# Optimization experiments

Hardware: AMD Instinct MI355X
Metric: run time of the kernel (lower is better)

## Reference

```python
import jax, jax.numpy as jnp
import numpy as np
import math

PS = 8          # patch_size
OUT_C = 16      # out_channels
D_MODEL = 64
P_STATE = 32
BANDLIMIT = 1.0
STEP_SCALE = 1.0  # dt1 reference rate


def _ln(x, g, b, eps=1e-5):
    mu = jnp.mean(x, -1, keepdims=True)
    var = jnp.mean((x - mu) ** 2, -1, keepdims=True)
    return (x - mu) * jax.lax.rsqrt(var + eps) * g + b


def _forward(x, W_embed, b_embed, g1, beta1, Lambda_re, Lambda_im, B_re, B_im,
             C_re, C_im, D, log_step, g2, beta2, W_enc, W_dec, g3, beta3, W_out, b_out):
    b, t, h, w = x.shape
    hp, wp = h // PS, w // PS
    n = hp * wp
    # patchify: [b,t,h,w] -> [b,t,n,ps*ps]
    xp = x.reshape(b, t, hp, PS, wp, PS).transpose(0, 1, 2, 4, 3, 5).reshape(b, t, n, PS * PS)
    xe = xp @ W_embed.T + b_embed                              # [b,t,n,d]
    u = xe.transpose(0, 2, 1, 3).reshape(b * n, t, D_MODEL)    # [(b n), t, d]

    # ---- S5Block: pre-norm -> diagonal SSM -> gelu + residual -> GEGLU FFN ----
    fx = _ln(u, g1, beta1)
    Lam = Lambda_re + 1j * Lambda_im                           # [P] complex eigenvalues
    step = STEP_SCALE * jnp.exp(log_step)                      # [P]
    Lbar = jnp.exp(Lam * step)                                 # ZOH: A_bar
    Bbar = ((Lbar - 1.0) / Lam)[:, None] * (B_re + 1j * B_im)  # ZOH: B_bar [P,d]
    # bandlimit mask on C (freqs = step*|Im(Lambda)|/(2pi) < bandlimit/2)
    freqs = step * jnp.abs(Lambda_im) / (2.0 * math.pi)
    mask = (freqs < BANDLIMIT * 0.5).astype(C_re.dtype)
    Cc = (C_re + 1j * C_im) * mask[None, :]                    # [d,P]

    Bu = jnp.einsum('ntd,pd->ntp', fx.astype(jnp.complex64), Bbar)   # [(bn),t,P]
    A = jnp.broadcast_to(Lbar.astype(jnp.complex64), (1, t, P_STATE))

    def comb(e1, e2):
        a1, b1 = e1
        a2, b2 = e2
        return a1 * a2, a2 * b1 + b2

    _, xs = jax.lax.associative_scan(comb, (A, Bu), axis=1)    # x_k = A*x_{k-1} + Bu_k (x_0 = 0)
    ys = jnp.einsum('ntp,dp->ntd', xs, Cc).real + fx * D       # y = Re(C x) + D u
    xb = jax.nn.gelu(ys, approximate=False) + fx

    fx2 = _ln(xb, g2, beta2)
    enc = fx2 @ W_enc.T                                        # [(bn),t,2d]
    a, gate = jnp.split(enc, 2, axis=-1)
    xb = (a * jax.nn.gelu(gate, approximate=False)) @ W_dec.T + fx2

    # ---- take last timestep, project, unpatchify ----
    x_last = xb[:, -1, :]                                      # [(bn), d]
    proj = _ln(x_last, g3, beta3) @ W_out.T + b_out            # [(bn), C*ps*ps]
    y = proj.reshape(b, hp, wp, OUT_C, PS, PS).transpose(0, 3, 1, 4, 2, 5).reshape(b, OUT_C, h, w)
    return y


def setup_inputs() -> dict:
    key = jax.random.key(0)
    ks = jax.random.split(key, 12)
    d, P, pp = D_MODEL, P_STATE, PS * PS
    return dict(
        x=jax.random.normal(ks[0], (8, 15, 480, 640), jnp.float32),
        W_embed=jax.random.normal(ks[1], (d, pp), jnp.float32) / math.sqrt(pp),
        b_embed=jnp.zeros((d,), jnp.float32),
        g1=jnp.ones((d,), jnp.float32), beta1=jnp.zeros((d,), jnp.float32),
        Lambda_re=-0.5 * jnp.ones((P,), jnp.float32),
        Lambda_im=math.pi * (1.0 + jnp.arange(P, dtype=jnp.float32)),
        B_re=jax.random.normal(ks[2], (P, d), jnp.float32) / math.sqrt(d),
        B_im=jax.random.normal(ks[3], (P, d), jnp.float32) / math.sqrt(d),
        C_re=jax.random.normal(ks[4], (d, P), jnp.float32) / math.sqrt(P),
        C_im=jax.random.normal(ks[5], (d, P), jnp.float32) / math.sqrt(P),
        D=jax.random.normal(ks[6], (d,), jnp.float32),
        log_step=jax.random.uniform(ks[7], (P,), jnp.float32, math.log(1e-3), math.log(1e-1)),
        g2=jnp.ones((d,), jnp.float32), beta2=jnp.zeros((d,), jnp.float32),
        W_enc=jax.random.normal(ks[8], (2 * d, d), jnp.float32) / math.sqrt(d),
        W_dec=jax.random.normal(ks[9], (d, d), jnp.float32) / math.sqrt(d),
        g3=jnp.ones((d,), jnp.float32), beta3=jnp.zeros((d,), jnp.float32),
        W_out=jax.random.normal(ks[10], (OUT_C * pp, d), jnp.float32) / math.sqrt(d),
        b_out=jnp.zeros((OUT_C * pp,), jnp.float32),
    )


def reference(x, W_embed, b_embed, g1, beta1, Lambda_re, Lambda_im, B_re, B_im,
              C_re, C_im, D, log_step, g2, beta2, W_enc, W_dec, g3, beta3, W_out, b_out):
    return _forward(x, W_embed, b_embed, g1, beta1, Lambda_re, Lambda_im, B_re, B_im,
                    C_re, C_im, D, log_step, g2, beta2, W_enc, W_dec, g3, beta3, W_out, b_out)
```

## Files before the change

kernel.cpp:

```cpp
#include <hip/hip_runtime.h>
#include <math.h>


typedef __attribute__((ext_vector_type(8))) short short8;
typedef __attribute__((ext_vector_type(4))) float f32x4;

#define MFMA16(a, b, c) __builtin_amdgcn_mfma_f32_16x16x32_bf16((a), (b), (c), 0, 0, 0)

__device__ __forceinline__ short f2bf(float f) {
  union { float f; unsigned u; } v; v.f = f;
  unsigned r = (v.u + 0x7fffu + ((v.u >> 16) & 1u)) >> 16;
  return (short)r;
}
__device__ __forceinline__ float geluf(float x) {
  return 0.5f * x * (1.0f + erff(x * 0.70710678118654752f));
}
__device__ __forceinline__ short8 packfrag(const f32x4& a, const f32x4& b) {
  short8 o;
  o[0] = f2bf(a[0]); o[1] = f2bf(a[1]); o[2] = f2bf(a[2]); o[3] = f2bf(a[3]);
  o[4] = f2bf(b[0]); o[5] = f2bf(b[1]); o[6] = f2bf(b[2]); o[7] = f2bf(b[3]);
  return o;
}
__device__ __forceinline__ int ecmap(int i, int m) {
  return (i >> 1) * 32 + (m >> 2) * 8 + (i & 1) * 4 + (m & 3);
}
__device__ __forceinline__ int swz(int b) {
  return b ^ (((b >> 2) ^ (b >> 6)) & 0x60) ^ (((b >> 3) ^ (b >> 9)) & 0x10);
}
__device__ __forceinline__ void bbar_factors(const float* Lre, const float* Lim,
                                             const float* lstep, int p,
                                             float& fre, float& fim) {
  float st = expf(lstep[p]);
  float lr = Lre[p], li = Lim[p];
  float er = expf(lr * st);
  float lbr = er * cosf(li * st), lbi = er * sinf(li * st);
  float u = lbr - 1.0f, v = lbi;
  float den = lr * lr + li * li;
  fre = (u * lr + v * li) / den;
  fim = (v * lr - u * li) / den;
}

__global__ __launch_bounds__(256) void k0_prep(
    const float* __restrict__ W_embed, const float* __restrict__ g1,
    const float* __restrict__ be1, const float* __restrict__ Lre,
    const float* __restrict__ Lim, const float* __restrict__ Bre,
    const float* __restrict__ Bim, const float* __restrict__ Cre,
    const float* __restrict__ Cim, const float* __restrict__ lstep,
    const float* __restrict__ W_enc, const float* __restrict__ W_dec,
    const float* __restrict__ W_out, short* __restrict__ wimg,
    float* __restrict__ bu0) {
  const int bid = blockIdx.x;
  if (bid == 44) {
    int q = threadIdx.x;
    if (q < 64) {
      int c = q >> 5, p = q & 31;
      float fre, fim; bbar_factors(Lre, Lim, lstep, p, fre, fim);
      float s = 0.f;
      for (int d = 0; d < 64; ++d) {
        float br = Bre[p * 64 + d], bi = Bim[p * 64 + d];
        float val = c ? (fre * bi + fim * br) : (fre * br - fim * bi);
        s += be1[d] * val;
      }
      bu0[q] = s;
    }
    return;
  }
  const int w = threadIdx.x >> 6, lane = threadIdx.x & 63;
  const int m = lane & 15, qd = lane >> 4;
  const int f = bid * 4 + w;
  short v[8];
  if (f < 8) {
    int i = f >> 1, kt = f & 1, chan = ecmap(i, m), k0 = kt * 32 + qd * 8;
#pragma unroll
    for (int j = 0; j < 8; ++j) v[j] = f2bf(W_embed[chan * 64 + k0 + j]);
  } else if (f < 16) {
    int fi = f - 8, i = fi >> 1, kt = fi & 1;
    int comp = i & 1, p = (i >> 1) * 16 + m, d0 = kt * 32 + qd * 8;
    float fre, fim; bbar_factors(Lre, Lim, lstep, p, fre, fim);
#pragma unroll
    for (int j = 0; j < 8; ++j) {
      int d = d0 + j;
      float br = Bre[p * 64 + d], bi = Bim[p * 64 + d];
      float val = comp ? (fre * bi + fim * br) : (fre * br - fim * bi);
      v[j] = f2bf(g1[d] * val);
    }
  } else if (f < 24) {
    int fi = f - 16, i = fi >> 1, kt = fi & 1, chan = ecmap(i, m);
#pragma unroll
    for (int j = 0; j < 8; ++j) {
      int comp = j >> 2, p = kt * 16 + qd * 4 + (j & 3);
      float stp = expf(lstep[p]);
      float fr = stp * fabsf(Lim[p]) * (1.0f / 6.28318530717958648f);
      float msk = (fr < 0.5f) ? 1.f : 0.f;
      float val = comp ? -Cim[chan * 32 + p] * msk : Cre[chan * 32 + p] * msk;
      v[j] = f2bf(val);
    }
  } else if (f < 40) {
    int fi = f - 24, i = fi >> 1, kt = fi & 1;
    int row = (i < 4) ? ecmap(i, m) : 64 + ecmap(i - 4, m);
#pragma unroll
    for (int j = 0; j < 8; ++j) v[j] = f2bf(W_enc[row * 64 + kt * 32 + qd * 8 + j]);
  } else if (f < 48) {
    int fi = f - 40, i = fi >> 1, kt = fi & 1, row = ecmap(i, m);
#pragma unroll
    for (int j = 0; j < 8; ++j) v[j] = f2bf(W_dec[row * 64 + kt * 32 + qd * 8 + j]);
  } else {
    int fi = f - 48, i = fi >> 1, kt = fi & 1, row = i * 16 + m;
#pragma unroll
    for (int j = 0; j < 8; ++j) v[j] = f2bf(W_out[row * 64 + kt * 32 + qd * 8 + j]);
  }
  short8 sv;
#pragma unroll
  for (int j = 0; j < 8; ++j) sv[j] = v[j];
  *(short8*)&wimg[(f * 64 + lane) * 8] = sv;
}

__global__ __launch_bounds__(256) void k1_fused(
    const float* __restrict__ x, const short* __restrict__ wimg_g,
    const float* __restrict__ bu0_g, const float* __restrict__ Lre,
    const float* __restrict__ Lim, const float* __restrict__ lstep,
    const float* __restrict__ g1, const float* __restrict__ be1,
    const float* __restrict__ bemb, const float* __restrict__ Dv,
    const float* __restrict__ g2, const float* __restrict__ be2,
    float* __restrict__ xlastT) {
  __shared__ __align__(16) char smem[49152];
#define WF(id) (*(const short8*)(smem + (id) * 1024 + lane * 16))

  const int tid = threadIdx.x;
  const int wv = tid >> 6, lane = tid & 63;
  const int s = lane & 15, qd = lane >> 4;

  float4 wreg[4];
  {
    const float4* src = (const float4*)wimg_g;
#pragma unroll
    for (int j = 0; j < 4; ++j) wreg[j] = src[j * 256 + tid];
  }

  int cb[4];
  f32x4 bec[4], bu0c[4];
#pragma unroll
  for (int nt = 0; nt < 4; ++nt) {
    cb[nt] = (nt >> 1) * 32 + qd * 8 + (nt & 1) * 4;
    bec[nt] = *(const f32x4*)(bemb + cb[nt]);
    bu0c[nt] = *(const f32x4*)(bu0_g + (nt & 1) * 32 + (nt >> 1) * 16 + qd * 4);
  }
  f32x4 lbr[2], lbi[2];
#pragma unroll
  for (int k = 0; k < 2; ++k)
#pragma unroll
    for (int r = 0; r < 4; ++r) {
      int p = k * 16 + qd * 4 + r;
      float st = expf(lstep[p]);
      float er = expf(Lre[p] * st);
      lbr[k][r] = er * cosf(Lim[p] * st);
      lbi[k][r] = er * sinf(Lim[p] * st);
    }

  int off[4];
#pragma unroll
  for (int j = 0; j < 4; ++j) {
    int L = (wv * 4 + j) * 1024 + lane * 16;
    int b = swz(L);
    int c = b >> 4;
    int r = c >> 7, p = (c >> 1) & 63, h = c & 1;
    int seq = blockIdx.x * 64 + p;
    int b_i = seq / 4800, pr = seq % 4800;
    int ph = pr / 80, pw = pr % 80;
    off[j] = ((b_i * 15) * 480 + ph * 8 + r) * 640 + pw * 8 + h * 4;
  }
  int rb[4];
#pragma unroll
  for (int kt = 0; kt < 2; ++kt)
#pragma unroll
    for (int h = 0; h < 2; ++h) {
      int b = (kt * 4 + qd) * 2048 + (wv * 16 + s) * 32 + h * 16;
      rb[kt * 2 + h] = swz(b);
    }

#define STAGE(bufofs, tt)                                                     \
  {                                                                           \
    const float* gsrc = x + (tt) * 307200;                                    \
    char* lb = smem + (bufofs) + wv * 4096;                                   \
    _Pragma("unroll") for (int j = 0; j < 4; ++j)                             \
        __builtin_amdgcn_global_load_lds(                                     \
            (const __attribute__((address_space(1))) void*)(gsrc + off[j]),   \
            (__attribute__((address_space(3))) void*)(lb + j * 1024),         \
            16, 0, 0);                                                        \
  }

  const int sbase = (blockIdx.x * 4 + wv) * 16;

  STAGE(16384, 0);
  STAGE(32768, 1);
  {
    float4* wdst = (float4*)smem;
#pragma unroll
    for (int j = 0; j < 4; ++j) wdst[j * 256 + tid] = wreg[j];
  }
  asm volatile("s_waitcnt vmcnt(0) lgkmcnt(0)" ::: "memory");
  __builtin_amdgcn_s_barrier();

  const f32x4 zf = {0.f, 0.f, 0.f, 0.f};
  f32x4 state[4] = {zf, zf, zf, zf};
  f32x4 xh[4];

  for (int t = 0; t < 15; ++t) {
    const char* bufr = smem + 16384 + ((t & 1) << 14);
    f32x4 vcur[4];
#pragma unroll
    for (int q = 0; q < 4; ++q) vcur[q] = *(const f32x4*)(bufr + rb[q]);
    asm volatile("s_waitcnt lgkmcnt(0)" ::: "memory");
    __builtin_amdgcn_s_barrier();
    if (t < 13) STAGE(16384 + ((t & 1) << 14), t + 2);

    short8 pa0 = packfrag(vcur[0], vcur[1]);
    short8 pa1 = packfrag(vcur[2], vcur[3]);
    f32x4 c1[4];
#pragma unroll
    for (int i = 0; i < 4; ++i) {
      f32x4 acc = MFMA16(WF(i * 2), pa0, zf);
      acc = MFMA16(WF(i * 2 + 1), pa1, acc);
      c1[i] = acc + bec[i];
    }
    float sm = 0.f, sq = 0.f;
#pragma unroll
    for (int nt = 0; nt < 4; ++nt)
#pragma unroll
      for (int i = 0; i < 4; ++i) { sm += c1[nt][i]; sq += c1[nt][i] * c1[nt][i]; }
    sm += __shfl_xor(sm, 16); sq += __shfl_xor(sq, 16);
    sm += __shfl_xor(sm, 32); sq += __shfl_xor(sq, 32);
    float mean = sm * 0.015625f;
    float rstd = rsqrtf(sq * 0.015625f - mean * mean + 1e-5f);
#pragma unroll
    for (int nt = 0; nt < 4; ++nt) xh[nt] = (c1[nt] - mean) * rstd;
    short8 xa0 = packfrag(xh[0], xh[1]);
    short8 xa1 = packfrag(xh[2], xh[3]);
#pragma unroll
    for (int k = 0; k < 2; ++k) {
      f32x4 re = state[2 * k], im = state[2 * k + 1];
      state[2 * k]     = lbr[k] * re - lbi[k] * im + bu0c[2 * k];
      state[2 * k + 1] = lbr[k] * im + lbi[k] * re + bu0c[2 * k + 1];
    }
#pragma unroll
    for (int i = 0; i < 4; ++i) {
      state[i] = MFMA16(WF(8 + i * 2), xa0, state[i]);
      state[i] = MFMA16(WF(8 + i * 2 + 1), xa1, state[i]);
    }

    if (t < 14) {
      if (t < 13) asm volatile("s_waitcnt vmcnt(4)" ::: "memory");
      else        asm volatile("s_waitcnt vmcnt(0)" ::: "memory");
      __builtin_amdgcn_s_barrier();
    }
  }
#undef STAGE

  __syncthreads();
  {
    float4 hf[8];
    const float4* src = (const float4*)(wimg_g + 16 * 512);
#pragma unroll
    for (int j = 0; j < 8; ++j) hf[j] = src[j * 256 + tid];
    float4* dst = (float4*)(smem + 16384);
#pragma unroll
    for (int j = 0; j < 8; ++j) dst[j * 256 + tid] = hf[j];
  }
  __syncthreads();

  f32x4 g1c[4], b1c[4], Dc[4], g2c[4], b2c[4];
#pragma unroll
  for (int nt = 0; nt < 4; ++nt) {
    g1c[nt] = *(const f32x4*)(g1 + cb[nt]);
    b1c[nt] = *(const f32x4*)(be1 + cb[nt]);
    Dc[nt] = *(const f32x4*)(Dv + cb[nt]);
    g2c[nt] = *(const f32x4*)(g2 + cb[nt]);
    b2c[nt] = *(const f32x4*)(be2 + cb[nt]);
  }
  f32x4 fxl[4];
#pragma unroll
  for (int nt = 0; nt < 4; ++nt) fxl[nt] = xh[nt] * g1c[nt] + b1c[nt];

  short8 xsa0 = packfrag(state[0], state[1]);
  short8 xsa1 = packfrag(state[2], state[3]);
  f32x4 xbv[4];
#pragma unroll
  for (int i = 0; i < 4; ++i) {
    f32x4 acc = fxl[i] * Dc[i];
    acc = MFMA16(WF(16 + i * 2), xsa0, acc);
    acc = MFMA16(WF(16 + i * 2 + 1), xsa1, acc);
#pragma unroll
    for (int r = 0; r < 4; ++r) xbv[i][r] = geluf(acc[r]) + fxl[i][r];
  }
  float sm2 = 0.f, sq2 = 0.f;
#pragma unroll
  for (int nt = 0; nt < 4; ++nt)
#pragma unroll
    for (int i = 0; i < 4; ++i) { sm2 += xbv[nt][i]; sq2 += xbv[nt][i] * xbv[nt][i]; }
  sm2 += __shfl_xor(sm2, 16); sq2 += __shfl_xor(sq2, 16);
  sm2 += __shfl_xor(sm2, 32); sq2 += __shfl_xor(sq2, 32);
  float mean2 = sm2 * 0.015625f;
  float rstd2 = rsqrtf(sq2 * 0.015625f - mean2 * mean2 + 1e-5f);
  f32x4 fx2[4];
#pragma unroll
  for (int nt = 0; nt < 4; ++nt)
    fx2[nt] = (xbv[nt] - mean2) * rstd2 * g2c[nt] + b2c[nt];

  short8 fa0 = packfrag(fx2[0], fx2[1]);
  short8 fa1 = packfrag(fx2[2], fx2[3]);
  f32x4 e[8];
#pragma unroll
  for (int i = 0; i < 8; ++i) {
    f32x4 acc = MFMA16(WF(24 + i * 2), fa0, zf);
    e[i] = MFMA16(WF(24 + i * 2 + 1), fa1, acc);
  }
  f32x4 hv[4];
#pragma unroll
  for (int nt = 0; nt < 4; ++nt)
#pragma unroll
    for (int i = 0; i < 4; ++i) hv[nt][i] = e[nt][i] * geluf(e[nt + 4][i]);

  short8 ha0 = packfrag(hv[0], hv[1]);
  short8 ha1 = packfrag(hv[2], hv[3]);
  f32x4 xo[4];
#pragma unroll
  for (int i = 0; i < 4; ++i) {
    f32x4 acc = fx2[i];
    acc = MFMA16(WF(40 + i * 2), ha0, acc);
    xo[i] = MFMA16(WF(40 + i * 2 + 1), ha1, acc);
  }
#pragma unroll
  for (int kt = 0; kt < 2; ++kt)
#pragma unroll
    for (int j = 0; j < 8; ++j)
      xlastT[(kt * 32 + qd * 8 + j) * 38400 + sbase + s] = xo[2 * kt + (j >> 2)][j & 3];
#undef WF
}

__global__ __launch_bounds__(256) void k2_head(
    const float* __restrict__ xlastT, const short* __restrict__ wout_img,
    const float* __restrict__ g3, const float* __restrict__ be3,
    const float* __restrict__ b_out, float* __restrict__ y) {
  __shared__ short wo[32 * 512];
  const int nqb = blockIdx.x & 3;
  const int mblk = blockIdx.x >> 2;
  {
    float4* dst = (float4*)wo;
    const float4* src = (const float4*)(wout_img + nqb * 32 * 512);
    for (int i = threadIdx.x; i < 2048; i += 256) dst[i] = src[i];
  }
  __syncthreads();
  const int wv = threadIdx.x >> 6, lane = threadIdx.x & 63;
  const int s = lane & 15, qd = lane >> 4;
  const int sbase = mblk * 64 + wv * 16;
  const int seq = sbase + s;
  const int nq0 = nqb * 256;

  float vals[2][8];
#pragma unroll
  for (int kt = 0; kt < 2; ++kt)
#pragma unroll
    for (int j = 0; j < 8; ++j)
      vals[kt][j] = xlastT[(kt * 32 + qd * 8 + j) * 38400 + seq];
  float sm = 0.f, sq = 0.f;
#pragma unroll
  for (int kt = 0; kt < 2; ++kt)
#pragma unroll
    for (int j = 0; j < 8; ++j) { sm += vals[kt][j]; sq += vals[kt][j] * vals[kt][j]; }
  sm += __shfl_xor(sm, 16); sq += __shfl_xor(sq, 16);
  sm += __shfl_xor(sm, 32); sq += __shfl_xor(sq, 32);
  float mean = sm * 0.015625f;
  float rstd = rsqrtf(sq * 0.015625f - mean * mean + 1e-5f);

  short8 zb[2];
#pragma unroll
  for (int kt = 0; kt < 2; ++kt) {
    f32x4 ga = *(const f32x4*)(g3 + kt * 32 + qd * 8);
    f32x4 gb = *(const f32x4*)(g3 + kt * 32 + qd * 8 + 4);
    f32x4 ba = *(const f32x4*)(be3 + kt * 32 + qd * 8);
    f32x4 bb = *(const f32x4*)(be3 + kt * 32 + qd * 8 + 4);
#pragma unroll
    for (int j = 0; j < 4; ++j) {
      zb[kt][j] = f2bf((vals[kt][j] - mean) * rstd * ga[j] + ba[j]);
      zb[kt][j + 4] = f2bf((vals[kt][j + 4] - mean) * rstd * gb[j] + bb[j]);
    }
  }
  const int bi2 = seq / 4800, prr = seq % 4800;
  const int phh = prr / 80, pww = prr % 80;
  const int obase = (bi2 * 16 * 480 + phh * 8) * 640 + pww * 8;

#pragma unroll
  for (int nt = 0; nt < 16; ++nt) {
    int o0 = nq0 + nt * 16 + qd * 4;
    f32x4 acc = *(const f32x4*)(b_out + o0);
    acc = MFMA16(*(const short8*)&wo[(nt * 2 + 0) * 512 + lane * 8], zb[0], acc);
    acc = MFMA16(*(const short8*)&wo[(nt * 2 + 1) * 512 + lane * 8], zb[1], acc);
    int c = o0 >> 6, pi = (o0 >> 3) & 7, pj = o0 & 7;
    *(f32x4*)&y[obase + c * 307200 + pi * 640 + pj] = acc;
  }
}

extern "C" void kernel_launch(void* const* d_in, const int* in_sizes, int n_in,
                              void* d_out, int out_size, void* d_ws, size_t ws_size,
                              hipStream_t stream) {
  const float* x       = (const float*)d_in[0];
  const float* W_embed = (const float*)d_in[1];
  const float* b_embed = (const float*)d_in[2];
  const float* g1      = (const float*)d_in[3];
  const float* beta1   = (const float*)d_in[4];
  const float* Lre     = (const float*)d_in[5];
  const float* Lim     = (const float*)d_in[6];
  const float* Bre     = (const float*)d_in[7];
  const float* Bim     = (const float*)d_in[8];
  const float* Cre     = (const float*)d_in[9];
  const float* Cim     = (const float*)d_in[10];
  const float* Dv      = (const float*)d_in[11];
  const float* lstep   = (const float*)d_in[12];
  const float* g2      = (const float*)d_in[13];
  const float* beta2   = (const float*)d_in[14];
  const float* W_enc   = (const float*)d_in[15];
  const float* W_dec   = (const float*)d_in[16];
  const float* g3      = (const float*)d_in[17];
  const float* beta3   = (const float*)d_in[18];
  const float* W_out   = (const float*)d_in[19];
  const float* b_out   = (const float*)d_in[20];
  float* y = (float*)d_out;

  short* wimg = (short*)d_ws;
  float* bu0 = (float*)((char*)d_ws + 176 * 1024);
  float* xlastT = (float*)((char*)d_ws + 180 * 1024);

  k0_prep<<<dim3(45), dim3(256), 0, stream>>>(W_embed, g1, beta1, Lre, Lim,
                                              Bre, Bim, Cre, Cim, lstep,
                                              W_enc, W_dec, W_out, wimg, bu0);
  k1_fused<<<dim3(600), dim3(256), 0, stream>>>(x, wimg, bu0, Lre, Lim, lstep,
                                                g1, beta1, b_embed, Dv, g2,
                                                beta2, xlastT);
  k2_head<<<dim3(2400), dim3(256), 0, stream>>>(xlastT, wimg + 48 * 512, g3,
                                                beta3, b_out, y);
}
```

Measured before the change: 342.3 us.

## Fuse final layernorm and output projection head into main SSM kernel

```diff
diff --git a/kernel.cpp b/kernel.cpp
--- a/kernel.cpp
+++ b/kernel.cpp
@@ -122,7 +122,8 @@
     const float* __restrict__ g1, const float* __restrict__ be1,
     const float* __restrict__ bemb, const float* __restrict__ Dv,
     const float* __restrict__ g2, const float* __restrict__ be2,
-    float* __restrict__ xlastT) {
+    const float* __restrict__ g3, const float* __restrict__ be3,
+    const float* __restrict__ b_out, float* __restrict__ y) {
   __shared__ __align__(16) char smem[49152];
 #define WF(id) (*(const short8*)(smem + (id) * 1024 + lane * 16))
 
@@ -329,75 +330,44 @@
     acc = MFMA16(WF(40 + i * 2), ha0, acc);
     xo[i] = MFMA16(WF(40 + i * 2 + 1), ha1, acc);
   }
-#pragma unroll
-  for (int kt = 0; kt < 2; ++kt)
-#pragma unroll
-    for (int j = 0; j < 8; ++j)
-      xlastT[(kt * 32 + qd * 8 + j) * 38400 + sbase + s] = xo[2 * kt + (j >> 2)][j & 3];
-#undef WF
-}
-
-__global__ __launch_bounds__(256) void k2_head(
-    const float* __restrict__ xlastT, const short* __restrict__ wout_img,
-    const float* __restrict__ g3, const float* __restrict__ be3,
-    const float* __restrict__ b_out, float* __restrict__ y) {
-  __shared__ short wo[32 * 512];
-  const int nqb = blockIdx.x & 3;
-  const int mblk = blockIdx.x >> 2;
-  {
-    float4* dst = (float4*)wo;
-    const float4* src = (const float4*)(wout_img + nqb * 32 * 512);
-    for (int i = threadIdx.x; i < 2048; i += 256) dst[i] = src[i];
-  }
-  __syncthreads();
-  const int wv = threadIdx.x >> 6, lane = threadIdx.x & 63;
-  const int s = lane & 15, qd = lane >> 4;
-  const int sbase = mblk * 64 + wv * 16;
+
+  float sm3 = 0.f, sq3 = 0.f;
+#pragma unroll
+  for (int nt = 0; nt < 4; ++nt)
+#pragma unroll
+    for (int i = 0; i < 4; ++i) { sm3 += xo[nt][i]; sq3 += xo[nt][i] * xo[nt][i]; }
+  sm3 += __shfl_xor(sm3, 16); sq3 += __shfl_xor(sq3, 16);
+  sm3 += __shfl_xor(sm3, 32); sq3 += __shfl_xor(sq3, 32);
+  float mean3 = sm3 * 0.015625f;
+  float rstd3 = rsqrtf(sq3 * 0.015625f - mean3 * mean3 + 1e-5f);
+  f32x4 z[4];
+#pragma unroll
+  for (int nt = 0; nt < 4; ++nt) {
+    f32x4 g3c = *(const f32x4*)(g3 + cb[nt]);
+    f32x4 b3c = *(const f32x4*)(be3 + cb[nt]);
+    z[nt] = (xo[nt] - mean3) * rstd3 * g3c + b3c;
+  }
+  short8 za = packfrag(z[0], z[1]);
+  short8 zb = packfrag(z[2], z[3]);
+
   const int seq = sbase + s;
-  const int nq0 = nqb * 256;
-
-  float vals[2][8];
-#pragma unroll
-  for (int kt = 0; kt < 2; ++kt)
-#pragma unroll
-    for (int j = 0; j < 8; ++j)
-      vals[kt][j] = xlastT[(kt * 32 + qd * 8 + j) * 38400 + seq];
-  float sm = 0.f, sq = 0.f;
-#pragma unroll
-  for (int kt = 0; kt < 2; ++kt)
-#pragma unroll
-    for (int j = 0; j < 8; ++j) { sm += vals[kt][j]; sq += vals[kt][j] * vals[kt][j]; }
-  sm += __shfl_xor(sm, 16); sq += __shfl_xor(sq, 16);
-  sm += __shfl_xor(sm, 32); sq += __shfl_xor(sq, 32);
-  float mean = sm * 0.015625f;
-  float rstd = rsqrtf(sq * 0.015625f - mean * mean + 1e-5f);
-
-  short8 zb[2];
-#pragma unroll
-  for (int kt = 0; kt < 2; ++kt) {
-    f32x4 ga = *(const f32x4*)(g3 + kt * 32 + qd * 8);
-    f32x4 gb = *(const f32x4*)(g3 + kt * 32 + qd * 8 + 4);
-    f32x4 ba = *(const f32x4*)(be3 + kt * 32 + qd * 8);
-    f32x4 bb = *(const f32x4*)(be3 + kt * 32 + qd * 8 + 4);
-#pragma unroll
-    for (int j = 0; j < 4; ++j) {
-      zb[kt][j] = f2bf((vals[kt][j] - mean) * rstd * ga[j] + ba[j]);
-      zb[kt][j + 4] = f2bf((vals[kt][j + 4] - mean) * rstd * gb[j] + bb[j]);
-    }
-  }
   const int bi2 = seq / 4800, prr = seq % 4800;
   const int phh = prr / 80, pww = prr % 80;
   const int obase = (bi2 * 16 * 480 + phh * 8) * 640 + pww * 8;
-
-#pragma unroll
-  for (int nt = 0; nt < 16; ++nt) {
-    int o0 = nq0 + nt * 16 + qd * 4;
+  const short* wob = wimg_g + 48 * 512;
+
+#pragma unroll 4
+  for (int ntg = 0; ntg < 64; ++ntg) {
+    short8 a0 = *(const short8*)&wob[(ntg * 2 + 0) * 512 + lane * 8];
+    short8 a1 = *(const short8*)&wob[(ntg * 2 + 1) * 512 + lane * 8];
+    int o0 = ntg * 16 + qd * 4;
     f32x4 acc = *(const f32x4*)(b_out + o0);
-    acc = MFMA16(*(const short8*)&wo[(nt * 2 + 0) * 512 + lane * 8], zb[0], acc);
-    acc = MFMA16(*(const short8*)&wo[(nt * 2 + 1) * 512 + lane * 8], zb[1], acc);
+    acc = MFMA16(a0, za, acc);
+    acc = MFMA16(a1, zb, acc);
     int c = o0 >> 6, pi = (o0 >> 3) & 7, pj = o0 & 7;
     *(f32x4*)&y[obase + c * 307200 + pi * 640 + pj] = acc;
   }
+#undef WF
 }
 
 extern "C" void kernel_launch(void* const* d_in, const int* in_sizes, int n_in,
@@ -428,14 +398,11 @@
 
   short* wimg = (short*)d_ws;
   float* bu0 = (float*)((char*)d_ws + 176 * 1024);
-  float* xlastT = (float*)((char*)d_ws + 180 * 1024);
 
   k0_prep<<<dim3(45), dim3(256), 0, stream>>>(W_embed, g1, beta1, Lre, Lim,
                                               Bre, Bim, Cre, Cim, lstep,
                                               W_enc, W_dec, W_out, wimg, bu0);
   k1_fused<<<dim3(600), dim3(256), 0, stream>>>(x, wimg, bu0, Lre, Lim, lstep,
                                                 g1, beta1, b_embed, Dv, g2,
-                                                beta2, xlastT);
-  k2_head<<<dim3(2400), dim3(256), 0, stream>>>(xlastT, wimg + 48 * 512, g3,
-                                                beta3, b_out, y);
-}
+                                                beta2, g3, beta3, b_out, y);
+}
```

Result: faster. 327.8 us (-4.2%).
